# Kernel optimization log

Measured on AMD Instinct MI355X. Metric: run time of the kernel, lower is better.

Reference implementation:

```python
import jax, jax.numpy as jnp
import numpy as np

HIDDEN = 2048
HEADS = 16
HEAD_DIM = HIDDEN // HEADS  # 128
SCALE = 1.0 / float(np.sqrt(HEAD_DIM))
B, S = 2, 2048


def setup_inputs() -> dict:
    key = jax.random.key(0)
    ks = jax.random.split(key, 5)
    return {
        "x": jax.random.normal(ks[0], (B, S, HIDDEN), dtype=jnp.float32),
        "q_w": jax.random.normal(ks[1], (HIDDEN, HIDDEN), dtype=jnp.float32) * (HIDDEN ** -0.5),
        "k_w": jax.random.normal(ks[2], (HEAD_DIM, HIDDEN), dtype=jnp.float32) * (HIDDEN ** -0.5),
        "v_w": jax.random.normal(ks[3], (HEAD_DIM, HIDDEN), dtype=jnp.float32) * (HIDDEN ** -0.5),
        "o_w": jax.random.normal(ks[4], (HIDDEN, HIDDEN), dtype=jnp.float32) * (HIDDEN ** -0.5),
    }


def reference(x, q_w, k_w, v_w, o_w):
    b, s, _ = x.shape
    # torch F.linear: x @ W^T with W [out, in]
    q = (x @ q_w.T).reshape(b, s, HEADS, HEAD_DIM).transpose(0, 2, 1, 3)  # [B,H,S,D]
    k = x @ k_w.T  # [B,S,D] single shared KV head
    v = x @ v_w.T  # [B,S,D]
    # scores: [B,H,S,S] -- explicit O(S^2) materialization as in the source
    scores = jnp.einsum('bhqd,bkd->bhqk', q, k) * SCALE
    # softmax in float32 then cast back (matches dtype=torch.float32 then type_as)
    attn = jax.nn.softmax(scores.astype(jnp.float32), axis=-1).astype(q.dtype)
    out = jnp.einsum('bhqk,bkd->bhqd', attn, v)  # [B,H,S,D]
    out = out.transpose(0, 2, 1, 3).reshape(b, s, HIDDEN)
    return out @ o_w.T
```

## Files before the change

### kernel.cpp

```cpp
#include <hip/hip_runtime.h>
#include <stdint.h>

#define HID 2048
#define DHEAD 128
#define SEQL 2048
#define C2 0.1275187981510609f
#define MOFF 8.0f

typedef __attribute__((ext_vector_type(4))) float f32x4;
typedef __attribute__((ext_vector_type(16))) float f32x16;
typedef __attribute__((ext_vector_type(8))) short s16x8;

__device__ __forceinline__ unsigned short bf16_rne(float f) {
  union { float f; unsigned u; } v; v.f = f;
  return (unsigned short)((v.u + 0x7FFFu + ((v.u >> 16) & 1u)) >> 16);
}

__device__ __forceinline__ void gload_lds16(const void* g, void* l) {
  __builtin_amdgcn_global_load_lds(
      (__attribute__((address_space(1))) unsigned int*)(void*)g,
      (__attribute__((address_space(3))) unsigned int*)l, 16, 0, 0);
}

__device__ __forceinline__ void cvt8(const float* __restrict__ in,
                                     unsigned short* __restrict__ out, int k) {
  const f32x4* p = (const f32x4*)in;
  f32x4 a = p[2 * k], b = p[2 * k + 1];
  union { s16x8 v; unsigned short s[8]; } o;
  o.s[0] = bf16_rne(a[0]); o.s[1] = bf16_rne(a[1]);
  o.s[2] = bf16_rne(a[2]); o.s[3] = bf16_rne(a[3]);
  o.s[4] = bf16_rne(b[0]); o.s[5] = bf16_rne(b[1]);
  o.s[6] = bf16_rne(b[2]); o.s[7] = bf16_rne(b[3]);
  ((s16x8*)out)[k] = o.v;
}

__global__ __launch_bounds__(256) void cvt_bf16_k(const float* __restrict__ in,
                                                  unsigned short* __restrict__ out,
                                                  int n8) {
  int i = blockIdx.x * 256 + threadIdx.x;
  if (i >= n8) return;
  cvt8(in, out, i);
}

__global__ __launch_bounds__(256) void cvt4_k(
    const float* __restrict__ s0, unsigned short* __restrict__ d0, int n0,
    const float* __restrict__ s1, unsigned short* __restrict__ d1, int n1,
    const float* __restrict__ s2, unsigned short* __restrict__ d2, int n2,
    const float* __restrict__ s3, unsigned short* __restrict__ d3, int n3) {
  int i = blockIdx.x * 256 + threadIdx.x;
  if (i < n0) { cvt8(s0, d0, i); return; }
  i -= n0;
  if (i < n1) { cvt8(s1, d1, i); return; }
  i -= n1;
  if (i < n2) { cvt8(s2, d2, i); return; }
  i -= n2;
  if (i < n3) { cvt8(s3, d3, i); return; }
}

__global__ __launch_bounds__(256) void cvt5_k(
    const float* __restrict__ s0, unsigned short* __restrict__ d0, int n0,
    const float* __restrict__ s1, unsigned short* __restrict__ d1, int n1,
    const float* __restrict__ s2, unsigned short* __restrict__ d2, int n2,
    const float* __restrict__ s3, unsigned short* __restrict__ d3, int n3,
    const float* __restrict__ s4, unsigned short* __restrict__ d4, int n4) {
  int i = blockIdx.x * 256 + threadIdx.x;
  if (i < n0) { cvt8(s0, d0, i); return; }
  i -= n0;
  if (i < n1) { cvt8(s1, d1, i); return; }
  i -= n1;
  if (i < n2) { cvt8(s2, d2, i); return; }
  i -= n2;
  if (i < n3) { cvt8(s3, d3, i); return; }
  i -= n3;
  if (i < n4) { cvt8(s4, d4, i); return; }
}

__device__ __forceinline__ void stage_tile512(const unsigned short* __restrict__ src,
                                              int ld, char* smem, int t) {
#pragma unroll
  for (int i = 0; i < 2; ++i) {
    int c = i * 512 + t;
    int row = c >> 3;
    int slot = c & 7;
    gload_lds16(src + row * ld + ((slot ^ (row & 7)) << 3),
                smem + (i * 512 + (t >> 6) * 64) * 16);
  }
}

template <int MODE>
__global__ __launch_bounds__(512, 4) void gemm_bt(
    const unsigned short* __restrict__ A, const unsigned short* __restrict__ Bw,
    void* __restrict__ Cout, int M, int N, int K,
    unsigned short* __restrict__ Kb, unsigned short* __restrict__ Vt) {
  __shared__ char As[2][16384];
  __shared__ char Bs[2][16384];
  int t = threadIdx.x;
  int lane = t & 63, w = t >> 6;
  int wm = w >> 2, wn = w & 3;
  int l15 = lane & 15, l4 = lane >> 4;

  int gdx = gridDim.x;
  int nwg = gdx * gridDim.y;
  int bid = blockIdx.y * gdx + blockIdx.x;
  int q8 = nwg >> 3;
  int swz = (bid & 7) * q8 + (bid >> 3);
  int tm = (swz / gdx) * 128, tn = (swz % gdx) * 128;

  f32x4 acc[4][2] = {};

  stage_tile512(A + tm * K, K, As[0], t);
  stage_tile512(Bw + tn * K, K, Bs[0], t);
  stage_tile512(A + tm * K + 64, K, As[1], t);
  stage_tile512(Bw + tn * K + 64, K, Bs[1], t);

  int nk = K >> 6;
  for (int ki = 0; ki < nk; ++ki) {
    int cur = ki & 1;
    if (ki < nk - 1) asm volatile("s_waitcnt vmcnt(4)" ::: "memory");
    else             asm volatile("s_waitcnt vmcnt(0)" ::: "memory");
    __builtin_amdgcn_sched_barrier(0);
    __builtin_amdgcn_s_barrier();

    const char* as = As[cur];
    const char* bs = Bs[cur];
    s16x8 af[4][2], bfr[2][2];
#pragma unroll
    for (int m = 0; m < 4; ++m)
#pragma unroll
      for (int kk = 0; kk < 2; ++kk) {
        int row = wm * 64 + m * 16 + l15;
        af[m][kk] = *(const s16x8*)(as + row * 128 + (((kk * 4 + l4) ^ (row & 7)) << 4));
      }
#pragma unroll
    for (int n = 0; n < 2; ++n)
#pragma unroll
      for (int kk = 0; kk < 2; ++kk) {
        int row = wn * 32 + n * 16 + l15;
        bfr[n][kk] = *(const s16x8*)(bs + row * 128 + (((kk * 4 + l4) ^ (row & 7)) << 4));
      }
    asm volatile("s_waitcnt lgkmcnt(0)" ::: "memory");
    __builtin_amdgcn_sched_barrier(0);
    __builtin_amdgcn_s_barrier();
    if (ki + 2 < nk) {
      stage_tile512(A + tm * K + (ki + 2) * 64, K, As[cur], t);
      stage_tile512(Bw + tn * K + (ki + 2) * 64, K, Bs[cur], t);
    }
    __builtin_amdgcn_s_setprio(1);
#pragma unroll
    for (int m = 0; m < 4; ++m)
#pragma unroll
      for (int n = 0; n < 2; ++n)
#pragma unroll
        for (int kk = 0; kk < 2; ++kk)
          acc[m][n] = __builtin_amdgcn_mfma_f32_16x16x32_bf16(af[m][kk], bfr[n][kk],
                                                              acc[m][n], 0, 0, 0);
    __builtin_amdgcn_s_setprio(0);
  }

#pragma unroll
  for (int m = 0; m < 4; ++m)
#pragma unroll
    for (int n = 0; n < 2; ++n) {
      int col = tn + wn * 32 + n * 16 + l15;
#pragma unroll
      for (int j = 0; j < 4; ++j) {
        int row = tm + wm * 64 + m * 16 + l4 * 4 + j;
        float v = acc[m][n][j];
        if (MODE == 1) {
          ((float*)Cout)[row * N + col] = v;
        } else {
          if (col < 2048) {
            ((unsigned short*)Cout)[row * 2048 + col] = bf16_rne(v);
          } else if (col < 2176) {
            Kb[row * 128 + (col - 2048)] = bf16_rne(v);
          } else {
            int d = col - 2176, bb = row >> 11, s = row & 2047;
            Vt[((bb * 128 + d) << 11) + s] = bf16_rne(v);
          }
        }
      }
    }
}

__global__ __launch_bounds__(256, 2) void attn_k(
    const unsigned short* __restrict__ Q, const unsigned short* __restrict__ Kb,
    const unsigned short* __restrict__ Vt, unsigned short* __restrict__ AO) {
  __shared__ char Ks[2][16384];
  __shared__ char Vs[16384];
  int t = threadIdx.x;
  int lane = t & 63, w = t >> 6;
  int l31 = lane & 31, lh = lane >> 5;
  int qt = blockIdx.x, bh = blockIdx.y;
  int b = bh >> 4, h = bh & 15;
  int qg = b * SEQL + qt * 128 + w * 32;

  s16x8 qf[8];
#pragma unroll
  for (int kc = 0; kc < 8; ++kc)
    qf[kc] = *(const s16x8*)(Q + (qg + l31) * HID + h * DHEAD + kc * 16 + lh * 8);

  union { s16x8 v; unsigned short s[8]; } one_;
#pragma unroll
  for (int i = 0; i < 8; ++i) one_.s[i] = 0x3F80;
  const s16x8 onesb = one_.v;

  f32x16 oacc[4] = {};
  f32x16 dacc = {};

#pragma unroll
  for (int i = 0; i < 4; ++i) {
    int c = i * 256 + t, row = c >> 4, slot = c & 15;
    gload_lds16(Kb + (b * SEQL + row) * DHEAD + ((slot ^ (row & 7)) << 3),
                Ks[0] + (i * 256 + w * 64) * 16);
  }
#pragma unroll
  for (int i = 0; i < 4; ++i) {
    int c = i * 256 + t, row = c >> 3, slot = c & 7;
    gload_lds16(Vt + (b * DHEAD + row) * SEQL + ((slot ^ (row & 7)) << 3),
                Vs + (i * 256 + w * 64) * 16);
  }
  asm volatile("s_waitcnt vmcnt(0)" ::: "memory");
  __builtin_amdgcn_s_barrier();

  for (int kv = 0; kv < SEQL; kv += 64) {
    int cur = (kv >> 6) & 1;
    bool more = (kv + 64 < SEQL);
    if (more) {
#pragma unroll
      for (int i = 0; i < 4; ++i) {
        int c = i * 256 + t, row = c >> 4, slot = c & 15;
        gload_lds16(Kb + (b * SEQL + kv + 64 + row) * DHEAD + ((slot ^ (row & 7)) << 3),
                    Ks[cur ^ 1] + (i * 256 + w * 64) * 16);
      }
    }

    const char* ks = Ks[cur];

    f32x16 s0 = {}, s1 = {};
    __builtin_amdgcn_s_setprio(1);
#pragma unroll
    for (int kc = 0; kc < 8; ++kc) {
      int slot = kc * 2 + lh;
      int r0 = l31, r1 = 32 + l31;
      s16x8 kf0 = *(const s16x8*)(ks + r0 * 256 + ((slot ^ (r0 & 7)) << 4));
      s16x8 kf1 = *(const s16x8*)(ks + r1 * 256 + ((slot ^ (r1 & 7)) << 4));
      s0 = __builtin_amdgcn_mfma_f32_32x32x16_bf16(kf0, qf[kc], s0, 0, 0, 0);
      s1 = __builtin_amdgcn_mfma_f32_32x32x16_bf16(kf1, qf[kc], s1, 0, 0, 0);
    }
    __builtin_amdgcn_s_setprio(0);

    s16x8 paf[4];
#pragma unroll
    for (int g = 0; g < 2; ++g)
#pragma unroll
      for (int half = 0; half < 2; ++half) {
        unsigned u[4];
#pragma unroll
        for (int i = 0; i < 4; ++i) {
          float pe = __builtin_amdgcn_exp2f(__builtin_fmaf(
              (g ? s1 : s0)[half * 8 + 2 * i], C2, -MOFF));
          float po = __builtin_amdgcn_exp2f(__builtin_fmaf(
              (g ? s1 : s0)[half * 8 + 2 * i + 1], C2, -MOFF));
          u[i] = (__builtin_bit_cast(unsigned, po) & 0xFFFF0000u) |
                 (__builtin_bit_cast(unsigned, pe) >> 16);
        }
        asm("v_permlane32_swap_b32 %0, %1" : "+v"(u[0]), "+v"(u[2]));
        asm("v_permlane32_swap_b32 %0, %1" : "+v"(u[1]), "+v"(u[3]));
        union { unsigned uu[4]; s16x8 v; } pk;
        pk.uu[0] = u[0]; pk.uu[1] = u[1]; pk.uu[2] = u[2]; pk.uu[3] = u[3];
        paf[g * 2 + half] = pk.v;
      }

    if (more) asm volatile("s_waitcnt vmcnt(4)" ::: "memory");
    else      asm volatile("s_waitcnt vmcnt(0)" ::: "memory");
    __builtin_amdgcn_sched_barrier(0);
    __builtin_amdgcn_s_barrier();

    __builtin_amdgcn_s_setprio(1);
#pragma unroll
    for (int kstep = 0; kstep < 4; ++kstep) {
#pragma unroll
      for (int dg = 0; dg < 4; ++dg) {
        int vrow = dg * 32 + l31;
        int slot = kstep * 2 + lh;
        s16x8 vf = *(const s16x8*)(Vs + vrow * 128 + ((slot ^ (vrow & 7)) << 4));
        oacc[dg] = __builtin_amdgcn_mfma_f32_32x32x16_bf16(paf[kstep], vf, oacc[dg], 0, 0, 0);
      }
      dacc = __builtin_amdgcn_mfma_f32_32x32x16_bf16(paf[kstep], onesb, dacc, 0, 0, 0);
    }
    __builtin_amdgcn_s_setprio(0);

    asm volatile("s_waitcnt vmcnt(0) lgkmcnt(0)" ::: "memory");
    __builtin_amdgcn_sched_barrier(0);
    __builtin_amdgcn_s_barrier();

    if (more) {
#pragma unroll
      for (int i = 0; i < 4; ++i) {
        int c = i * 256 + t, row = c >> 3, slot = c & 7;
        gload_lds16(Vt + (b * DHEAD + row) * SEQL + kv + 64 + ((slot ^ (row & 7)) << 3),
                    Vs + (i * 256 + w * 64) * 16);
      }
    }
  }

  float inv[16];
#pragma unroll
  for (int r = 0; r < 16; ++r) inv[r] = 1.f / dacc[r];
#pragma unroll
  for (int dg = 0; dg < 4; ++dg)
#pragma unroll
    for (int r = 0; r < 16; ++r) {
      int qi = (r & 3) + 8 * (r >> 2) + 4 * lh;
      AO[(qg + qi) * HID + h * DHEAD + dg * 32 + l31] = bf16_rne(oacc[dg][r] * inv[r]);
    }
}

extern "C" void kernel_launch(void* const* d_in, const int* in_sizes, int n_in,
                              void* d_out, int out_size, void* d_ws, size_t ws_size,
                              hipStream_t stream) {
  const float* x  = (const float*)d_in[0];
  const float* qw = (const float*)d_in[1];
  const float* kw = (const float*)d_in[2];
  const float* vw = (const float*)d_in[3];
  const float* ow = (const float*)d_in[4];

  char* ws = (char*)d_ws;
  unsigned short* xb   = (unsigned short*)(ws);
  unsigned short* qwb  = (unsigned short*)(ws + 16777216);
  unsigned short* kvwb = (unsigned short*)(ws + 25165824);
  unsigned short* Qb   = (unsigned short*)(ws + 26214400);
  unsigned short* Kbuf = (unsigned short*)(ws + 42991616);
  unsigned short* Vtb  = (unsigned short*)(ws + 44040192);
  unsigned short* AOb  = xb;

  bool big = ws_size >= 54525953ull;
  unsigned short* owb = big ? (unsigned short*)(ws + 46137344) : qwb;

  if (big) {
    cvt5_k<<<8448, 256, 0, stream>>>(x, xb, 1048576, qw, qwb, 524288,
                                     kw, kvwb, 32768, vw, kvwb + 262144, 32768,
                                     ow, owb, 524288);
  } else {
    cvt4_k<<<6400, 256, 0, stream>>>(x, xb, 1048576, qw, qwb, 524288,
                                     kw, kvwb, 32768, vw, kvwb + 262144, 32768);
  }

  gemm_bt<0><<<dim3(18, 32), 512, 0, stream>>>(xb, qwb, Qb, 4096, 2304, 2048, Kbuf, Vtb);
  if (!big) {
    cvt_bf16_k<<<2048, 256, 0, stream>>>(ow, owb, 524288);
  }
  attn_k<<<dim3(16, 32), 256, 0, stream>>>(Qb, Kbuf, Vtb, AOb);
  gemm_bt<1><<<dim3(16, 32), 512, 0, stream>>>(AOb, owb, d_out, 4096, 2048, 2048,
                                               nullptr, nullptr);
}
```

Before: 192.8 us.

## Give each attention wave two query groups to reuse K/V fragments

The attention kernel now runs 128 threads (2 waves) per block, and each wave handles 64 query rows as two 32-row groups. Every K and V fragment read from LDS therefore feeds two MFMAs, halving LDS traffic per unit of compute. In exchange each wave holds roughly twice as many accumulator and Q registers, fewer waves are resident, and the V-load wait was simplified to a full vmcnt(0). Scheduling barriers were also added in the GEMM and attention loops.

```diff
diff --git a/kernel.cpp b/kernel.cpp
--- a/kernel.cpp
+++ b/kernel.cpp
@@ -145,6 +145,7 @@
       stage_tile512(A + tm * K + (ki + 2) * 64, K, As[cur], t);
       stage_tile512(Bw + tn * K + (ki + 2) * 64, K, Bs[cur], t);
     }
+    __builtin_amdgcn_sched_barrier(0);
     __builtin_amdgcn_s_setprio(1);
 #pragma unroll
     for (int m = 0; m < 4; ++m)
@@ -182,7 +183,7 @@
     }
 }
 
-__global__ __launch_bounds__(256, 2) void attn_k(
+__global__ __launch_bounds__(128, 1) void attn_k(
     const unsigned short* __restrict__ Q, const unsigned short* __restrict__ Kb,
     const unsigned short* __restrict__ Vt, unsigned short* __restrict__ AO) {
   __shared__ char Ks[2][16384];
@@ -192,34 +193,38 @@
   int l31 = lane & 31, lh = lane >> 5;
   int qt = blockIdx.x, bh = blockIdx.y;
   int b = bh >> 4, h = bh & 15;
-  int qg = b * SEQL + qt * 128 + w * 32;
-
-  s16x8 qf[8];
-#pragma unroll
-  for (int kc = 0; kc < 8; ++kc)
-    qf[kc] = *(const s16x8*)(Q + (qg + l31) * HID + h * DHEAD + kc * 16 + lh * 8);
+  int qg0 = b * SEQL + qt * 128 + w * 64;
+
+  s16x8 qf[2][8];
+#pragma unroll
+  for (int g = 0; g < 2; ++g)
+#pragma unroll
+    for (int kc = 0; kc < 8; ++kc)
+      qf[g][kc] = *(const s16x8*)(Q + (qg0 + g * 32 + l31) * HID + h * DHEAD +
+                                  kc * 16 + lh * 8);
 
   union { s16x8 v; unsigned short s[8]; } one_;
 #pragma unroll
   for (int i = 0; i < 8; ++i) one_.s[i] = 0x3F80;
   const s16x8 onesb = one_.v;
 
-  f32x16 oacc[4] = {};
-  f32x16 dacc = {};
-
-#pragma unroll
-  for (int i = 0; i < 4; ++i) {
-    int c = i * 256 + t, row = c >> 4, slot = c & 15;
+  f32x16 oacc[2][4] = {};
+  f32x16 dacc[2] = {};
+
+#pragma unroll
+  for (int i = 0; i < 8; ++i) {
+    int c = i * 128 + t, row = c >> 4, slot = c & 15;
     gload_lds16(Kb + (b * SEQL + row) * DHEAD + ((slot ^ (row & 7)) << 3),
-                Ks[0] + (i * 256 + w * 64) * 16);
-  }
-#pragma unroll
-  for (int i = 0; i < 4; ++i) {
-    int c = i * 256 + t, row = c >> 3, slot = c & 7;
+                Ks[0] + (i * 128 + w * 64) * 16);
+  }
+#pragma unroll
+  for (int i = 0; i < 8; ++i) {
+    int c = i * 128 + t, row = c >> 3, slot = c & 7;
     gload_lds16(Vt + (b * DHEAD + row) * SEQL + ((slot ^ (row & 7)) << 3),
-                Vs + (i * 256 + w * 64) * 16);
+                Vs + (i * 128 + w * 64) * 16);
   }
   asm volatile("s_waitcnt vmcnt(0)" ::: "memory");
+  __builtin_amdgcn_sched_barrier(0);
   __builtin_amdgcn_s_barrier();
 
   for (int kv = 0; kv < SEQL; kv += 64) {
@@ -227,52 +232,57 @@
     bool more = (kv + 64 < SEQL);
     if (more) {
 #pragma unroll
-      for (int i = 0; i < 4; ++i) {
-        int c = i * 256 + t, row = c >> 4, slot = c & 15;
+      for (int i = 0; i < 8; ++i) {
+        int c = i * 128 + t, row = c >> 4, slot = c & 15;
         gload_lds16(Kb + (b * SEQL + kv + 64 + row) * DHEAD + ((slot ^ (row & 7)) << 3),
-                    Ks[cur ^ 1] + (i * 256 + w * 64) * 16);
-      }
-    }
+                    Ks[cur ^ 1] + (i * 128 + w * 64) * 16);
+      }
+    }
+    __builtin_amdgcn_sched_barrier(0);
 
     const char* ks = Ks[cur];
 
-    f32x16 s0 = {}, s1 = {};
+    f32x16 s00 = {}, s01 = {}, s10 = {}, s11 = {};
     __builtin_amdgcn_s_setprio(1);
 #pragma unroll
     for (int kc = 0; kc < 8; ++kc) {
       int slot = kc * 2 + lh;
-      int r0 = l31, r1 = 32 + l31;
-      s16x8 kf0 = *(const s16x8*)(ks + r0 * 256 + ((slot ^ (r0 & 7)) << 4));
-      s16x8 kf1 = *(const s16x8*)(ks + r1 * 256 + ((slot ^ (r1 & 7)) << 4));
-      s0 = __builtin_amdgcn_mfma_f32_32x32x16_bf16(kf0, qf[kc], s0, 0, 0, 0);
-      s1 = __builtin_amdgcn_mfma_f32_32x32x16_bf16(kf1, qf[kc], s1, 0, 0, 0);
+      int xr = (l31 & 7);
+      s16x8 kf0 = *(const s16x8*)(ks + l31 * 256 + ((slot ^ xr) << 4));
+      s16x8 kf1 = *(const s16x8*)(ks + (32 + l31) * 256 + ((slot ^ xr) << 4));
+      s00 = __builtin_amdgcn_mfma_f32_32x32x16_bf16(kf0, qf[0][kc], s00, 0, 0, 0);
+      s10 = __builtin_amdgcn_mfma_f32_32x32x16_bf16(kf0, qf[1][kc], s10, 0, 0, 0);
+      s01 = __builtin_amdgcn_mfma_f32_32x32x16_bf16(kf1, qf[0][kc], s01, 0, 0, 0);
+      s11 = __builtin_amdgcn_mfma_f32_32x32x16_bf16(kf1, qf[1][kc], s11, 0, 0, 0);
     }
     __builtin_amdgcn_s_setprio(0);
 
-    s16x8 paf[4];
+    s16x8 paf[2][4];
 #pragma unroll
     for (int g = 0; g < 2; ++g)
 #pragma unroll
-      for (int half = 0; half < 2; ++half) {
-        unsigned u[4];
-#pragma unroll
-        for (int i = 0; i < 4; ++i) {
-          float pe = __builtin_amdgcn_exp2f(__builtin_fmaf(
-              (g ? s1 : s0)[half * 8 + 2 * i], C2, -MOFF));
-          float po = __builtin_amdgcn_exp2f(__builtin_fmaf(
-              (g ? s1 : s0)[half * 8 + 2 * i + 1], C2, -MOFF));
-          u[i] = (__builtin_bit_cast(unsigned, po) & 0xFFFF0000u) |
-                 (__builtin_bit_cast(unsigned, pe) >> 16);
+      for (int kg = 0; kg < 2; ++kg)
+#pragma unroll
+        for (int half = 0; half < 2; ++half) {
+          const f32x16& sv = g ? (kg ? s11 : s10) : (kg ? s01 : s00);
+          unsigned u[4];
+#pragma unroll
+          for (int i = 0; i < 4; ++i) {
+            float pe = __builtin_amdgcn_exp2f(__builtin_fmaf(
+                sv[half * 8 + 2 * i], C2, -MOFF));
+            float po = __builtin_amdgcn_exp2f(__builtin_fmaf(
+                sv[half * 8 + 2 * i + 1], C2, -MOFF));
+            u[i] = (__builtin_bit_cast(unsigned, po) & 0xFFFF0000u) |
+                   (__builtin_bit_cast(unsigned, pe) >> 16);
+          }
+          asm("v_permlane32_swap_b32 %0, %1" : "+v"(u[0]), "+v"(u[2]));
+          asm("v_permlane32_swap_b32 %0, %1" : "+v"(u[1]), "+v"(u[3]));
+          union { unsigned uu[4]; s16x8 v; } pk;
+          pk.uu[0] = u[0]; pk.uu[1] = u[1]; pk.uu[2] = u[2]; pk.uu[3] = u[3];
+          paf[g][kg * 2 + half] = pk.v;
         }
-        asm("v_permlane32_swap_b32 %0, %1" : "+v"(u[0]), "+v"(u[2]));
-        asm("v_permlane32_swap_b32 %0, %1" : "+v"(u[1]), "+v"(u[3]));
-        union { unsigned uu[4]; s16x8 v; } pk;
-        pk.uu[0] = u[0]; pk.uu[1] = u[1]; pk.uu[2] = u[2]; pk.uu[3] = u[3];
-        paf[g * 2 + half] = pk.v;
-      }
-
-    if (more) asm volatile("s_waitcnt vmcnt(4)" ::: "memory");
-    else      asm volatile("s_waitcnt vmcnt(0)" ::: "memory");
+
+    asm volatile("s_waitcnt vmcnt(0)" ::: "memory");
     __builtin_amdgcn_sched_barrier(0);
     __builtin_amdgcn_s_barrier();
 
@@ -284,36 +294,45 @@
         int vrow = dg * 32 + l31;
         int slot = kstep * 2 + lh;
         s16x8 vf = *(const s16x8*)(Vs + vrow * 128 + ((slot ^ (vrow & 7)) << 4));
-        oacc[dg] = __builtin_amdgcn_mfma_f32_32x32x16_bf16(paf[kstep], vf, oacc[dg], 0, 0, 0);
-      }
-      dacc = __builtin_amdgcn_mfma_f32_32x32x16_bf16(paf[kstep], onesb, dacc, 0, 0, 0);
+        oacc[0][dg] = __builtin_amdgcn_mfma_f32_32x32x16_bf16(paf[0][kstep], vf,
+                                                              oacc[0][dg], 0, 0, 0);
+        oacc[1][dg] = __builtin_amdgcn_mfma_f32_32x32x16_bf16(paf[1][kstep], vf,
+                                                              oacc[1][dg], 0, 0, 0);
+      }
+      dacc[0] = __builtin_amdgcn_mfma_f32_32x32x16_bf16(paf[0][kstep], onesb, dacc[0], 0, 0, 0);
+      dacc[1] = __builtin_amdgcn_mfma_f32_32x32x16_bf16(paf[1][kstep], onesb, dacc[1], 0, 0, 0);
     }
     __builtin_amdgcn_s_setprio(0);
 
-    asm volatile("s_waitcnt vmcnt(0) lgkmcnt(0)" ::: "memory");
+    asm volatile("s_waitcnt lgkmcnt(0)" ::: "memory");
     __builtin_amdgcn_sched_barrier(0);
     __builtin_amdgcn_s_barrier();
 
     if (more) {
 #pragma unroll
-      for (int i = 0; i < 4; ++i) {
-        int c = i * 256 + t, row = c >> 3, slot = c & 7;
+      for (int i = 0; i < 8; ++i) {
+        int c = i * 128 + t, row = c >> 3, slot = c & 7;
         gload_lds16(Vt + (b * DHEAD + row) * SEQL + kv + 64 + ((slot ^ (row & 7)) << 3),
-                    Vs + (i * 256 + w * 64) * 16);
-      }
-    }
-  }
-
-  float inv[16];
-#pragma unroll
-  for (int r = 0; r < 16; ++r) inv[r] = 1.f / dacc[r];
-#pragma unroll
-  for (int dg = 0; dg < 4; ++dg)
-#pragma unroll
-    for (int r = 0; r < 16; ++r) {
-      int qi = (r & 3) + 8 * (r >> 2) + 4 * lh;
-      AO[(qg + qi) * HID + h * DHEAD + dg * 32 + l31] = bf16_rne(oacc[dg][r] * inv[r]);
-    }
+                    Vs + (i * 128 + w * 64) * 16);
+      }
+    }
+    __builtin_amdgcn_sched_barrier(0);
+  }
+
+#pragma unroll
+  for (int g = 0; g < 2; ++g) {
+    float inv[16];
+#pragma unroll
+    for (int r = 0; r < 16; ++r) inv[r] = 1.f / dacc[g][r];
+#pragma unroll
+    for (int dg = 0; dg < 4; ++dg)
+#pragma unroll
+      for (int r = 0; r < 16; ++r) {
+        int qi = (r & 3) + 8 * (r >> 2) + 4 * lh;
+        AO[(qg0 + g * 32 + qi) * HID + h * DHEAD + dg * 32 + l31] =
+            bf16_rne(oacc[g][dg][r] * inv[r]);
+      }
+  }
 }
 
 extern "C" void kernel_launch(void* const* d_in, const int* in_sizes, int n_in,
@@ -350,7 +369,7 @@
   if (!big) {
     cvt_bf16_k<<<2048, 256, 0, stream>>>(ow, owb, 524288);
   }
-  attn_k<<<dim3(16, 32), 256, 0, stream>>>(Qb, Kbuf, Vtb, AOb);
+  attn_k<<<dim3(16, 32), 128, 0, stream>>>(Qb, Kbuf, Vtb, AOb);
   gemm_bt<1><<<dim3(16, 32), 512, 0, stream>>>(AOb, owb, d_out, 4096, 2048, 2048,
                                                nullptr, nullptr);
 }
```

Result: slower. 220.4 us (+14.3%).
